# Performance work log

Measured on AMD Instinct MI355X. Metric: run time of the kernel, lower is better.

## Reference

```python
import jax, jax.numpy as jnp
from jax import lax
import numpy as np

T, B, H = 128, 4096, 64

def setup_inputs() -> dict:
    key = jax.random.key(0)
    ks = jax.random.split(key, 7)
    s = 1.0 / np.sqrt(H)
    Hseq = jax.random.normal(ks[0], (T, B, H), dtype=jnp.float32)
    # PyTorch nn.GRU params: weight_ih_l0 [3H,H], weight_hh_l0 [3H,H], biases [3H]; gate order r,z,n
    W_ih = jax.random.uniform(ks[1], (3 * H, H), jnp.float32, -s, s)
    W_hh = jax.random.uniform(ks[2], (3 * H, H), jnp.float32, -s, s)
    b_ih = jax.random.uniform(ks[3], (3 * H,), jnp.float32, -s, s)
    b_hh = jax.random.uniform(ks[4], (3 * H,), jnp.float32, -s, s)
    W_out = jax.random.uniform(ks[5], (1, H), jnp.float32, -s, s)
    b_out = jax.random.uniform(ks[6], (1,), jnp.float32, -s, s)
    return {"Hseq": Hseq, "W_ih": W_ih, "W_hh": W_hh, "b_ih": b_ih, "b_hh": b_hh, "W_out": W_out, "b_out": b_out}

def reference(Hseq, W_ih, W_hh, b_ih, b_hh, W_out, b_out):
    # Precompute all input-side gate projections in one big GEMM: [T,B,3H]
    x_gates = jnp.einsum('tbh,gh->tbg', Hseq, W_ih) + b_ih

    def step(h, xg):
        hg = h @ W_hh.T + b_hh                     # [B,3H]
        xr, xz, xn = jnp.split(xg, 3, axis=-1)
        hr, hz, hn = jnp.split(hg, 3, axis=-1)
        r = jax.nn.sigmoid(xr + hr)
        z = jax.nn.sigmoid(xz + hz)
        n = jnp.tanh(xn + r * hn)
        h_new = (1.0 - z) * n + z * h
        return h_new, None

    h0 = jnp.zeros(Hseq.shape[1:], Hseq.dtype)      # [B,H], PyTorch default h0=0
    last, _ = lax.scan(step, h0, x_gates)           # last hidden == Y[-1]
    return (last @ W_out.T + b_out).squeeze(-1)     # [B]
```

## Files before the change

kernel.cpp:

```cpp
#include <hip/hip_runtime.h>
#include <stdint.h>

#define TT 128
#define BB 4096
#define HH 64
#define BC 16
#define HSTR 72

typedef __attribute__((ext_vector_type(8))) short bf16x8;
typedef __attribute__((ext_vector_type(4))) float f32x4;

static __device__ __forceinline__ short f2bf(float f) {
  uint32_t u = __builtin_bit_cast(uint32_t, f);
  u += 0x7fffu + ((u >> 16) & 1u);
  return (short)(u >> 16);
}
static __device__ __forceinline__ uint32_t cvtpk(float a, float b) {
  uint32_t r;
  asm("v_cvt_pk_bf16_f32 %0, %1, %2" : "=v"(r) : "v"(a), "v"(b));
  return r;
}
static __device__ __forceinline__ float rcpf(float x) { return __builtin_amdgcn_rcpf(x); }
static __device__ __forceinline__ float sigm(float x) { return rcpf(1.0f + __expf(-x)); }
static __device__ __forceinline__ float tanhf_fast(float x) {
  float e = __expf(2.0f * x);
  return 1.0f - 2.0f * rcpf(e + 1.0f);
}

static __device__ __forceinline__ void block_sync_lds() {
  asm volatile("" ::: "memory");
  asm volatile("s_waitcnt lgkmcnt(0)" ::: "memory");
  __builtin_amdgcn_s_barrier();
  asm volatile("" ::: "memory");
}

__global__ __launch_bounds__(256) void gru_fused(
    const float* __restrict__ Hseq, const float* __restrict__ W_ih,
    const float* __restrict__ W_hh, const float* __restrict__ b_ih,
    const float* __restrict__ b_hh, const float* __restrict__ W_out,
    const float* __restrict__ b_out, float* __restrict__ out) {
  __shared__ __align__(16) short hsh[2][BC][HSTR];
  __shared__ float psum[4][BC];

  const int tid = threadIdx.x;
  const int w   = tid >> 6;
  const int l   = tid & 63;
  const int llo = l & 15;
  const int lhi = l >> 4;
  const int k0  = lhi * 8;
  const int bbase = blockIdx.x * BC;

  bf16x8 wih[3][2], whh[3][2];
#pragma unroll
  for (int c = 0; c < 3; ++c) {
    const int grow = 64 * c + 16 * w + llo;
#pragma unroll
    for (int hf = 0; hf < 2; ++hf) {
      const float* p = &W_ih[grow * 64 + hf * 32 + k0];
      const float* q = &W_hh[grow * 64 + hf * 32 + k0];
      bf16x8 a, b;
#pragma unroll
      for (int i = 0; i < 8; ++i) { a[i] = f2bf(p[i]); b[i] = f2bf(q[i]); }
      wih[c][hf] = a;
      whh[c][hf] = b;
    }
  }

  f32x4 biasR, biasZ, biasXN, biasHN;
#pragma unroll
  for (int r = 0; r < 4; ++r) {
    const int j = 16 * w + 4 * lhi + r;
    biasR[r]  = b_ih[j] + b_hh[j];
    biasZ[r]  = b_ih[64 + j] + b_hh[64 + j];
    biasXN[r] = b_ih[128 + j];
    biasHN[r] = b_hh[128 + j];
  }

  for (int i = tid; i < (BC * HSTR) / 2; i += 256) ((int*)hsh[0])[i] = 0;

  const float* xroot = Hseq + (size_t)(bbase + llo) * HH + k0;
  f32x4 xq0, xq1, xq2, xq3;
  {
    const f32x4* pv = (const f32x4*)xroot;
    xq0 = pv[0]; xq1 = pv[1]; xq2 = pv[8]; xq3 = pv[9];
  }
  f32x4 cR, cZ, cXN;
  {
    union { uint32_t u[4]; bf16x8 v; } x0, x1;
    x0.u[0] = cvtpk(xq0[0], xq0[1]); x0.u[1] = cvtpk(xq0[2], xq0[3]);
    x0.u[2] = cvtpk(xq1[0], xq1[1]); x0.u[3] = cvtpk(xq1[2], xq1[3]);
    x1.u[0] = cvtpk(xq2[0], xq2[1]); x1.u[1] = cvtpk(xq2[2], xq2[3]);
    x1.u[2] = cvtpk(xq3[0], xq3[1]); x1.u[3] = cvtpk(xq3[2], xq3[3]);
    cR  = __builtin_amdgcn_mfma_f32_16x16x32_bf16(wih[0][0], x0.v, biasR, 0, 0, 0);
    cR  = __builtin_amdgcn_mfma_f32_16x16x32_bf16(wih[0][1], x1.v, cR, 0, 0, 0);
    cZ  = __builtin_amdgcn_mfma_f32_16x16x32_bf16(wih[1][0], x0.v, biasZ, 0, 0, 0);
    cZ  = __builtin_amdgcn_mfma_f32_16x16x32_bf16(wih[1][1], x1.v, cZ, 0, 0, 0);
    cXN = __builtin_amdgcn_mfma_f32_16x16x32_bf16(wih[2][0], x0.v, biasXN, 0, 0, 0);
    cXN = __builtin_amdgcn_mfma_f32_16x16x32_bf16(wih[2][1], x1.v, cXN, 0, 0, 0);
  }
  {
    const f32x4* pv = (const f32x4*)(xroot + (size_t)BB * HH);
    xq0 = pv[0]; xq1 = pv[1]; xq2 = pv[8]; xq3 = pv[9];
  }

  f32x4 hfp = {0.f, 0.f, 0.f, 0.f};
  block_sync_lds();

  for (int t = 0; t < TT; ++t) {
    const int buf = t & 1;
    const bf16x8 hb0 = *(const bf16x8*)&hsh[buf][llo][k0];
    const bf16x8 hb1 = *(const bf16x8*)&hsh[buf][llo][k0 + 32];
    f32x4 aR  = __builtin_amdgcn_mfma_f32_16x16x32_bf16(whh[0][0], hb0, cR, 0, 0, 0);
    aR        = __builtin_amdgcn_mfma_f32_16x16x32_bf16(whh[0][1], hb1, aR, 0, 0, 0);
    f32x4 aZ  = __builtin_amdgcn_mfma_f32_16x16x32_bf16(whh[1][0], hb0, cZ, 0, 0, 0);
    aZ        = __builtin_amdgcn_mfma_f32_16x16x32_bf16(whh[1][1], hb1, aZ, 0, 0, 0);
    f32x4 aHN = __builtin_amdgcn_mfma_f32_16x16x32_bf16(whh[2][0], hb0, biasHN, 0, 0, 0);
    aHN       = __builtin_amdgcn_mfma_f32_16x16x32_bf16(whh[2][1], hb1, aHN, 0, 0, 0);
    const f32x4 aXN = cXN;

#pragma unroll
    for (int r = 0; r < 4; ++r) {
      const float rr = sigm(aR[r]);
      const float zz = sigm(aZ[r]);
      const float nn = tanhf_fast(aXN[r] + rr * aHN[r]);
      hfp[r] = nn + zz * (hfp[r] - nn);
    }
    uint2 pk;
    pk.x = cvtpk(hfp[0], hfp[1]);
    pk.y = cvtpk(hfp[2], hfp[3]);
    *(uint2*)&hsh[buf ^ 1][llo][16 * w + 4 * lhi] = pk;

    union { uint32_t u[4]; bf16x8 v; } x0, x1;
    x0.u[0] = cvtpk(xq0[0], xq0[1]); x0.u[1] = cvtpk(xq0[2], xq0[3]);
    x0.u[2] = cvtpk(xq1[0], xq1[1]); x0.u[3] = cvtpk(xq1[2], xq1[3]);
    x1.u[0] = cvtpk(xq2[0], xq2[1]); x1.u[1] = cvtpk(xq2[2], xq2[3]);
    x1.u[2] = cvtpk(xq3[0], xq3[1]); x1.u[3] = cvtpk(xq3[2], xq3[3]);
    cR  = __builtin_amdgcn_mfma_f32_16x16x32_bf16(wih[0][0], x0.v, biasR, 0, 0, 0);
    cR  = __builtin_amdgcn_mfma_f32_16x16x32_bf16(wih[0][1], x1.v, cR, 0, 0, 0);
    cZ  = __builtin_amdgcn_mfma_f32_16x16x32_bf16(wih[1][0], x0.v, biasZ, 0, 0, 0);
    cZ  = __builtin_amdgcn_mfma_f32_16x16x32_bf16(wih[1][1], x1.v, cZ, 0, 0, 0);
    cXN = __builtin_amdgcn_mfma_f32_16x16x32_bf16(wih[2][0], x0.v, biasXN, 0, 0, 0);
    cXN = __builtin_amdgcn_mfma_f32_16x16x32_bf16(wih[2][1], x1.v, cXN, 0, 0, 0);
    {
      const int tn = (t + 2 < TT) ? t + 2 : TT - 1;
      const f32x4* pv = (const f32x4*)(xroot + (size_t)tn * BB * HH);
      xq0 = pv[0]; xq1 = pv[1]; xq2 = pv[8]; xq3 = pv[9];
    }
    block_sync_lds();
  }

  {
    float part = 0.f;
#pragma unroll
    for (int r = 0; r < 4; ++r) part += hfp[r] * W_out[16 * w + 4 * lhi + r];
    part += __shfl_xor(part, 16);
    part += __shfl_xor(part, 32);
    if (lhi == 0) psum[w][llo] = part;
  }
  block_sync_lds();
  if (tid < BC)
    out[bbase + tid] = psum[0][tid] + psum[1][tid] + psum[2][tid] + psum[3][tid] + b_out[0];
}

extern "C" void kernel_launch(void* const* d_in, const int* in_sizes, int n_in,
                              void* d_out, int out_size, void* d_ws, size_t ws_size,
                              hipStream_t stream) {
  (void)in_sizes; (void)n_in; (void)d_ws; (void)ws_size; (void)out_size;
  const float* Hseq  = (const float*)d_in[0];
  const float* W_ih  = (const float*)d_in[1];
  const float* W_hh  = (const float*)d_in[2];
  const float* b_ih  = (const float*)d_in[3];
  const float* b_hh  = (const float*)d_in[4];
  const float* W_out = (const float*)d_in[5];
  const float* b_out = (const float*)d_in[6];
  float* out = (float*)d_out;
  gru_fused<<<BB / BC, 256, 0, stream>>>(Hseq, W_ih, W_hh, b_ih, b_hh, W_out, b_out, out);
}
```

Baseline: 83.40 us.

## Halve batch rows per block and deepen input prefetch with 2x unrolled steps

Cuts the batch chunk per block from 16 to 8 rows, which doubles the grid so each CU holds two blocks whose serial recurrences can interleave and hide MFMA, LDS and barrier latency. The 16-wide MFMA tiles are kept, so lanes 8-15 compute duplicate rows and half the matrix work is redundant. The time loop is also unrolled by two with two register sets of prefetched inputs. This raises the prefetch distance to three steps and issues the global loads before the recurrent MFMAs. The cost is more register pressure and twice the total MFMA and input-load traffic.

```diff
diff --git a/kernel.cpp b/kernel.cpp
--- a/kernel.cpp
+++ b/kernel.cpp
@@ -4,7 +4,7 @@
 #define TT 128
 #define BB 4096
 #define HH 64
-#define BC 16
+#define BC 8
 #define HSTR 72
 
 typedef __attribute__((ext_vector_type(8))) short bf16x8;
@@ -39,8 +39,8 @@
     const float* __restrict__ W_hh, const float* __restrict__ b_ih,
     const float* __restrict__ b_hh, const float* __restrict__ W_out,
     const float* __restrict__ b_out, float* __restrict__ out) {
-  __shared__ __align__(16) short hsh[2][BC][HSTR];
-  __shared__ float psum[4][BC];
+  __shared__ __align__(16) short hsh[2][16][HSTR];
+  __shared__ float psum[4][16];
 
   const int tid = threadIdx.x;
   const int w   = tid >> 6;
@@ -49,6 +49,7 @@
   const int lhi = l >> 4;
   const int k0  = lhi * 8;
   const int bbase = blockIdx.x * BC;
+  const int brow  = llo & (BC - 1);
 
   bf16x8 wih[3][2], whh[3][2];
 #pragma unroll
@@ -76,21 +77,19 @@
     biasHN[r] = b_hh[128 + j];
   }
 
-  for (int i = tid; i < (BC * HSTR) / 2; i += 256) ((int*)hsh[0])[i] = 0;
+  for (int i = tid; i < (16 * HSTR) / 2; i += 256) ((int*)hsh[0])[i] = 0;
 
-  const float* xroot = Hseq + (size_t)(bbase + llo) * HH + k0;
-  f32x4 xq0, xq1, xq2, xq3;
+  const float* xroot = Hseq + (size_t)(bbase + brow) * HH + k0;
+
+  f32x4 cR, cZ, cXN;
   {
     const f32x4* pv = (const f32x4*)xroot;
-    xq0 = pv[0]; xq1 = pv[1]; xq2 = pv[8]; xq3 = pv[9];
-  }
-  f32x4 cR, cZ, cXN;
-  {
+    f32x4 q0 = pv[0], q1 = pv[1], q2 = pv[8], q3 = pv[9];
     union { uint32_t u[4]; bf16x8 v; } x0, x1;
-    x0.u[0] = cvtpk(xq0[0], xq0[1]); x0.u[1] = cvtpk(xq0[2], xq0[3]);
-    x0.u[2] = cvtpk(xq1[0], xq1[1]); x0.u[3] = cvtpk(xq1[2], xq1[3]);
-    x1.u[0] = cvtpk(xq2[0], xq2[1]); x1.u[1] = cvtpk(xq2[2], xq2[3]);
-    x1.u[2] = cvtpk(xq3[0], xq3[1]); x1.u[3] = cvtpk(xq3[2], xq3[3]);
+    x0.u[0] = cvtpk(q0[0], q0[1]); x0.u[1] = cvtpk(q0[2], q0[3]);
+    x0.u[2] = cvtpk(q1[0], q1[1]); x0.u[3] = cvtpk(q1[2], q1[3]);
+    x1.u[0] = cvtpk(q2[0], q2[1]); x1.u[1] = cvtpk(q2[2], q2[3]);
+    x1.u[2] = cvtpk(q3[0], q3[1]); x1.u[3] = cvtpk(q3[2], q3[3]);
     cR  = __builtin_amdgcn_mfma_f32_16x16x32_bf16(wih[0][0], x0.v, biasR, 0, 0, 0);
     cR  = __builtin_amdgcn_mfma_f32_16x16x32_bf16(wih[0][1], x1.v, cR, 0, 0, 0);
     cZ  = __builtin_amdgcn_mfma_f32_16x16x32_bf16(wih[1][0], x0.v, biasZ, 0, 0, 0);
@@ -98,56 +97,66 @@
     cXN = __builtin_amdgcn_mfma_f32_16x16x32_bf16(wih[2][0], x0.v, biasXN, 0, 0, 0);
     cXN = __builtin_amdgcn_mfma_f32_16x16x32_bf16(wih[2][1], x1.v, cXN, 0, 0, 0);
   }
+  f32x4 xqA0, xqA1, xqA2, xqA3, xqB0, xqB1, xqB2, xqB3;
   {
-    const f32x4* pv = (const f32x4*)(xroot + (size_t)BB * HH);
-    xq0 = pv[0]; xq1 = pv[1]; xq2 = pv[8]; xq3 = pv[9];
+    const f32x4* pa = (const f32x4*)(xroot + (size_t)1 * BB * HH);
+    xqA0 = pa[0]; xqA1 = pa[1]; xqA2 = pa[8]; xqA3 = pa[9];
+    const f32x4* pb = (const f32x4*)(xroot + (size_t)2 * BB * HH);
+    xqB0 = pb[0]; xqB1 = pb[1]; xqB2 = pb[8]; xqB3 = pb[9];
   }
 
   f32x4 hfp = {0.f, 0.f, 0.f, 0.f};
   block_sync_lds();
 
-  for (int t = 0; t < TT; ++t) {
-    const int buf = t & 1;
-    const bf16x8 hb0 = *(const bf16x8*)&hsh[buf][llo][k0];
-    const bf16x8 hb1 = *(const bf16x8*)&hsh[buf][llo][k0 + 32];
-    f32x4 aR  = __builtin_amdgcn_mfma_f32_16x16x32_bf16(whh[0][0], hb0, cR, 0, 0, 0);
-    aR        = __builtin_amdgcn_mfma_f32_16x16x32_bf16(whh[0][1], hb1, aR, 0, 0, 0);
-    f32x4 aZ  = __builtin_amdgcn_mfma_f32_16x16x32_bf16(whh[1][0], hb0, cZ, 0, 0, 0);
-    aZ        = __builtin_amdgcn_mfma_f32_16x16x32_bf16(whh[1][1], hb1, aZ, 0, 0, 0);
-    f32x4 aHN = __builtin_amdgcn_mfma_f32_16x16x32_bf16(whh[2][0], hb0, biasHN, 0, 0, 0);
-    aHN       = __builtin_amdgcn_mfma_f32_16x16x32_bf16(whh[2][1], hb1, aHN, 0, 0, 0);
-    const f32x4 aXN = cXN;
+#define STEP(RB, WB, XQ0, XQ1, XQ2, XQ3, TN)                                  \
+  {                                                                           \
+    const bf16x8 hb0 = *(const bf16x8*)&hsh[RB][llo][k0];                     \
+    const bf16x8 hb1 = *(const bf16x8*)&hsh[RB][llo][k0 + 32];                \
+                                   \
+    union { uint32_t u[4]; bf16x8 v; } x0, x1;                                \
+    x0.u[0] = cvtpk(XQ0[0], XQ0[1]); x0.u[1] = cvtpk(XQ0[2], XQ0[3]);         \
+    x0.u[2] = cvtpk(XQ1[0], XQ1[1]); x0.u[3] = cvtpk(XQ1[2], XQ1[3]);         \
+    x1.u[0] = cvtpk(XQ2[0], XQ2[1]); x1.u[1] = cvtpk(XQ2[2], XQ2[3]);         \
+    x1.u[2] = cvtpk(XQ3[0], XQ3[1]); x1.u[3] = cvtpk(XQ3[2], XQ3[3]);         \
+    {                                                                         \
+      const int tn = (TN) < TT ? (TN) : (TT - 1);                             \
+      const f32x4* pv = (const f32x4*)(xroot + (size_t)tn * BB * HH);         \
+      XQ0 = pv[0]; XQ1 = pv[1]; XQ2 = pv[8]; XQ3 = pv[9];                     \
+    }                                                                         \
+                         \
+    f32x4 aR  = __builtin_amdgcn_mfma_f32_16x16x32_bf16(whh[0][0], hb0, cR, 0, 0, 0);   \
+    aR        = __builtin_amdgcn_mfma_f32_16x16x32_bf16(whh[0][1], hb1, aR, 0, 0, 0);   \
+    f32x4 aZ  = __builtin_amdgcn_mfma_f32_16x16x32_bf16(whh[1][0], hb0, cZ, 0, 0, 0);   \
+    aZ        = __builtin_amdgcn_mfma_f32_16x16x32_bf16(whh[1][1], hb1, aZ, 0, 0, 0);   \
+    f32x4 aHN = __builtin_amdgcn_mfma_f32_16x16x32_bf16(whh[2][0], hb0, biasHN, 0, 0, 0); \
+    aHN       = __builtin_amdgcn_mfma_f32_16x16x32_bf16(whh[2][1], hb1, aHN, 0, 0, 0);  \
+                                 \
+    _Pragma("unroll")                                                         \
+    for (int r = 0; r < 4; ++r) {                                             \
+      const float rr = sigm(aR[r]);                                           \
+      const float zz = sigm(aZ[r]);                                           \
+      const float nn = tanhf_fast(cXN[r] + rr * aHN[r]);                      \
+      hfp[r] = nn + zz * (hfp[r] - nn);                                       \
+    }                                                                         \
+    uint2 pk;                                                                 \
+    pk.x = cvtpk(hfp[0], hfp[1]);                                             \
+    pk.y = cvtpk(hfp[2], hfp[3]);                                             \
+    *(uint2*)&hsh[WB][llo][16 * w + 4 * lhi] = pk;                            \
+                 \
+    cR  = __builtin_amdgcn_mfma_f32_16x16x32_bf16(wih[0][0], x0.v, biasR, 0, 0, 0);     \
+    cR  = __builtin_amdgcn_mfma_f32_16x16x32_bf16(wih[0][1], x1.v, cR, 0, 0, 0);        \
+    cZ  = __builtin_amdgcn_mfma_f32_16x16x32_bf16(wih[1][0], x0.v, biasZ, 0, 0, 0);     \
+    cZ  = __builtin_amdgcn_mfma_f32_16x16x32_bf16(wih[1][1], x1.v, cZ, 0, 0, 0);        \
+    cXN = __builtin_amdgcn_mfma_f32_16x16x32_bf16(wih[2][0], x0.v, biasXN, 0, 0, 0);    \
+    cXN = __builtin_amdgcn_mfma_f32_16x16x32_bf16(wih[2][1], x1.v, cXN, 0, 0, 0);       \
+    block_sync_lds();                                                         \
+  }
 
-#pragma unroll
-    for (int r = 0; r < 4; ++r) {
-      const float rr = sigm(aR[r]);
-      const float zz = sigm(aZ[r]);
-      const float nn = tanhf_fast(aXN[r] + rr * aHN[r]);
-      hfp[r] = nn + zz * (hfp[r] - nn);
-    }
-    uint2 pk;
-    pk.x = cvtpk(hfp[0], hfp[1]);
-    pk.y = cvtpk(hfp[2], hfp[3]);
-    *(uint2*)&hsh[buf ^ 1][llo][16 * w + 4 * lhi] = pk;
-
-    union { uint32_t u[4]; bf16x8 v; } x0, x1;
-    x0.u[0] = cvtpk(xq0[0], xq0[1]); x0.u[1] = cvtpk(xq0[2], xq0[3]);
-    x0.u[2] = cvtpk(xq1[0], xq1[1]); x0.u[3] = cvtpk(xq1[2], xq1[3]);
-    x1.u[0] = cvtpk(xq2[0], xq2[1]); x1.u[1] = cvtpk(xq2[2], xq2[3]);
-    x1.u[2] = cvtpk(xq3[0], xq3[1]); x1.u[3] = cvtpk(xq3[2], xq3[3]);
-    cR  = __builtin_amdgcn_mfma_f32_16x16x32_bf16(wih[0][0], x0.v, biasR, 0, 0, 0);
-    cR  = __builtin_amdgcn_mfma_f32_16x16x32_bf16(wih[0][1], x1.v, cR, 0, 0, 0);
-    cZ  = __builtin_amdgcn_mfma_f32_16x16x32_bf16(wih[1][0], x0.v, biasZ, 0, 0, 0);
-    cZ  = __builtin_amdgcn_mfma_f32_16x16x32_bf16(wih[1][1], x1.v, cZ, 0, 0, 0);
-    cXN = __builtin_amdgcn_mfma_f32_16x16x32_bf16(wih[2][0], x0.v, biasXN, 0, 0, 0);
-    cXN = __builtin_amdgcn_mfma_f32_16x16x32_bf16(wih[2][1], x1.v, cXN, 0, 0, 0);
-    {
-      const int tn = (t + 2 < TT) ? t + 2 : TT - 1;
-      const f32x4* pv = (const f32x4*)(xroot + (size_t)tn * BB * HH);
-      xq0 = pv[0]; xq1 = pv[1]; xq2 = pv[8]; xq3 = pv[9];
-    }
-    block_sync_lds();
+  for (int t = 0; t < TT; t += 2) {
+    STEP(0, 1, xqA0, xqA1, xqA2, xqA3, t + 3);
+    STEP(1, 0, xqB0, xqB1, xqB2, xqB3, t + 4);
   }
+#undef STEP
 
   {
     float part = 0.f;
```

After: 125.1 us. 1.5x slower.
